# Performance work log

Hardware: AMD Instinct MI355X
Metric: run time of the kernel (lower is better)

The kernel has to match this reference:

```python
import jax, jax.numpy as jnp
import numpy as np

N = 8192        # nodes
D_IN = 256      # in_dims
D_OUT = 32      # out_dims (assignment clusters)


def setup_inputs() -> dict:
    key = jax.random.key(0)
    k1, k2, k3 = jax.random.split(key, 3)
    main_feat = jax.random.normal(k1, (N, D_IN), dtype=jnp.float32)
    main_adj = jax.random.uniform(k2, (N, N), dtype=jnp.float32)
    W = jax.random.normal(k3, (D_IN, D_OUT), dtype=jnp.float32) * (1.0 / np.sqrt(D_IN))
    b = jnp.zeros((D_OUT,), dtype=jnp.float32)
    return {"main_feat": main_feat, "main_adj": main_adj, "W": W, "b": b}


def reference(main_feat, main_adj, W, b):
    # GraphConvolution: support = X @ W ; out = A @ support + b   -> [N, D_OUT]
    support = main_feat @ W
    assign = main_adj @ support + b
    # softmax over the NODE axis (dim 0), matching F.softmax(main_assign, 0)
    assign = jax.nn.softmax(assign, axis=0)
    # pooling: raw_emb = assign^T @ X  -> [D_OUT, D_IN]
    raw_emb = assign.T @ main_feat
    return raw_emb
```

## Files before the change

### kernel.cpp

```cpp
#include <hip/hip_runtime.h>
#include <stdint.h>

#define NN   8192
#define DIN  256
#define DOUT 32

typedef short bf16x8 __attribute__((ext_vector_type(8)));
typedef float f32x16 __attribute__((ext_vector_type(16)));

union BF8 { uint32_t u[4]; bf16x8 v; };

__device__ __forceinline__ void split_pair(float a, float b, uint32_t& hp, uint32_t& lp) {
    uint32_t ua = __float_as_uint(a), ub = __float_as_uint(b);
    hp = (ua >> 16) | (ub & 0xffff0000u);
    float la = a - __uint_as_float(ua & 0xffff0000u);
    float lb = b - __uint_as_float(ub & 0xffff0000u);
    lp = (__float_as_uint(la) >> 16) | (__float_as_uint(lb) & 0xffff0000u);
}

__global__ __launch_bounds__(256) void k1_support(
    const float* __restrict__ X, const float* __restrict__ W,
    unsigned short* __restrict__ hi_frag, unsigned short* __restrict__ lo_frag)
{
    __shared__ float Xs[32 * 256];
    int t = threadIdx.x;
    int kbase = blockIdx.x * 32;

    const float4* Xg = (const float4*)(X + (size_t)kbase * DIN);
    float4* Xs4 = (float4*)Xs;
#pragma unroll
    for (int p = 0; p < 8; ++p) Xs4[p * 256 + t] = Xg[p * 256 + t];
    __syncthreads();

    int c = t & 31;
    int q = t >> 5;
    int kb2  = q >> 2;
    int half = (q >> 1) & 1;
    int j4   = q & 1;
    int krow0 = kb2 * 16 + half * 8 + j4 * 4;

    float acc[4] = {0.f, 0.f, 0.f, 0.f};
    for (int d = 0; d < 256; ++d) {
        float w = W[d * 32 + c];
#pragma unroll
        for (int jj = 0; jj < 4; ++jj)
            acc[jj] += Xs[(krow0 + jj) * 256 + d] * w;
    }

    uint32_t h01, l01, h23, l23;
    split_pair(acc[0], acc[1], h01, l01);
    split_pair(acc[2], acc[3], h23, l23);

    int ks = (kbase >> 4) + kb2;
    size_t elembase = (size_t)ks * 512 + (size_t)(half * 32 + c) * 8 + j4 * 4;
    *(uint2*)(hi_frag + elembase) = make_uint2(h01, h23);
    *(uint2*)(lo_frag + elembase) = make_uint2(l01, l23);
}

__global__ __launch_bounds__(256) void k2_logits(
    const float* __restrict__ adj,
    const unsigned short* __restrict__ hi_frag,
    const unsigned short* __restrict__ lo_frag,
    float* __restrict__ part)
{
    int t = threadIdx.x;
    int lane = t & 63, wv = t >> 6;
    int row_tile = blockIdx.x * 128 + wv * 32;
    int r  = lane & 31;
    int hs = lane >> 5;

    const float* arow = adj + (size_t)(row_tile + r) * NN + blockIdx.y * 512 + hs * 8;
    const unsigned short* hp = hi_frag + (size_t)blockIdx.y * 32 * 512 + lane * 8;
    const unsigned short* lp = lo_frag + (size_t)blockIdx.y * 32 * 512 + lane * 8;

    f32x16 acc;
#pragma unroll
    for (int i = 0; i < 16; ++i) acc[i] = 0.f;

#pragma unroll 4
    for (int s = 0; s < 32; ++s) {
        float4 a0 = *(const float4*)arow;
        float4 a1 = *(const float4*)(arow + 4);
        BF8 bh, bl, ah, al;
        bh.v = *(const bf16x8*)hp;
        bl.v = *(const bf16x8*)lp;
        split_pair(a0.x, a0.y, ah.u[0], al.u[0]);
        split_pair(a0.z, a0.w, ah.u[1], al.u[1]);
        split_pair(a1.x, a1.y, ah.u[2], al.u[2]);
        split_pair(a1.z, a1.w, ah.u[3], al.u[3]);
        acc = __builtin_amdgcn_mfma_f32_32x32x16_bf16(ah.v, bh.v, acc, 0, 0, 0);
        acc = __builtin_amdgcn_mfma_f32_32x32x16_bf16(ah.v, bl.v, acc, 0, 0, 0);
        acc = __builtin_amdgcn_mfma_f32_32x32x16_bf16(al.v, bh.v, acc, 0, 0, 0);
        arow += 16; hp += 512; lp += 512;
    }

    float* pdst = part + (size_t)blockIdx.y * (NN * DOUT);
#pragma unroll
    for (int reg = 0; reg < 16; ++reg) {
        int rt = (reg & 3) + 8 * (reg >> 2) + 4 * hs;
        pdst[(size_t)(row_tile + rt) * 32 + r] = acc[reg];
    }
}

__global__ __launch_bounds__(256) void k3a_sum_max(
    const float* __restrict__ part, float* __restrict__ logits_sum,
    float* __restrict__ Mpart)
{
    __shared__ float red[256 * 4];
    int t = threadIdx.x;
    size_t base4 = (size_t)blockIdx.x * 1024;

    float mx[4] = {-3.4e38f, -3.4e38f, -3.4e38f, -3.4e38f};
#pragma unroll
    for (int k = 0; k < 4; ++k) {
        size_t f = base4 + k * 256 + t;
        float4 v = ((const float4*)part)[f];
#pragma unroll
        for (int p = 1; p < 16; ++p) {
            float4 u = ((const float4*)(part + (size_t)p * NN * DOUT))[f];
            v.x += u.x; v.y += u.y; v.z += u.z; v.w += u.w;
        }
        ((float4*)logits_sum)[f] = v;
        mx[0] = fmaxf(mx[0], v.x); mx[1] = fmaxf(mx[1], v.y);
        mx[2] = fmaxf(mx[2], v.z); mx[3] = fmaxf(mx[3], v.w);
    }
#pragma unroll
    for (int j = 0; j < 4; ++j) red[t * 4 + j] = mx[j];
    __syncthreads();
    for (int s = 128; s >= 8; s >>= 1) {
        if (t < s)
#pragma unroll
            for (int j = 0; j < 4; ++j)
                red[t * 4 + j] = fmaxf(red[t * 4 + j], red[(t + s) * 4 + j]);
        __syncthreads();
    }
    if (t < 8)
#pragma unroll
        for (int j = 0; j < 4; ++j)
            Mpart[blockIdx.x * 32 + t * 4 + j] = red[t * 4 + j];
}

__global__ __launch_bounds__(256) void k3b_exp_sum(
    const float* __restrict__ logits_sum, const float* __restrict__ Mpart,
    float* __restrict__ e_buf, float* __restrict__ Spart)
{
    __shared__ float Ms[32];
    __shared__ float red[256 * 4];
    int t = threadIdx.x;

    if (t < 32) {
        float m = -3.4e38f;
        for (int g = 0; g < 64; ++g) m = fmaxf(m, Mpart[g * 32 + t]);
        Ms[t] = m;
    }
    __syncthreads();

    int g = t & 7;
    float m0 = Ms[4 * g], m1 = Ms[4 * g + 1], m2 = Ms[4 * g + 2], m3 = Ms[4 * g + 3];
    size_t base4 = (size_t)blockIdx.x * 1024;
    float sm[4] = {0.f, 0.f, 0.f, 0.f};
#pragma unroll
    for (int k = 0; k < 4; ++k) {
        size_t f = base4 + k * 256 + t;
        float4 v = ((const float4*)logits_sum)[f];
        v.x = __expf(v.x - m0); v.y = __expf(v.y - m1);
        v.z = __expf(v.z - m2); v.w = __expf(v.w - m3);
        ((float4*)e_buf)[f] = v;
        sm[0] += v.x; sm[1] += v.y; sm[2] += v.z; sm[3] += v.w;
    }
#pragma unroll
    for (int j = 0; j < 4; ++j) red[t * 4 + j] = sm[j];
    __syncthreads();
    for (int s = 128; s >= 8; s >>= 1) {
        if (t < s)
#pragma unroll
            for (int j = 0; j < 4; ++j)
                red[t * 4 + j] += red[(t + s) * 4 + j];
        __syncthreads();
    }
    if (t < 8)
#pragma unroll
        for (int j = 0; j < 4; ++j)
            Spart[blockIdx.x * 32 + t * 4 + j] = red[t * 4 + j];
}

__global__ __launch_bounds__(256) void k4_pool(
    const float* __restrict__ X, const float* __restrict__ e_buf,
    const float* __restrict__ Spart, float* __restrict__ p4)
{
    __shared__ float Xs[8 * 256];
    __shared__ float As[8 * 32];
    __shared__ float invS[32];
    int t = threadIdx.x;
    int c = t & 31, dg = t >> 5;
    int ibase = blockIdx.x * 64;

    if (t < 32) {
        float s = 0.f;
        for (int g = 0; g < 64; ++g) s += Spart[g * 32 + t];
        invS[t] = 1.0f / s;
    }

    float acc[32];
#pragma unroll
    for (int i = 0; i < 32; ++i) acc[i] = 0.f;

    for (int rnd = 0; rnd < 8; ++rnd) {
        __syncthreads();
        const float4* Xg = (const float4*)(X + (size_t)(ibase + rnd * 8) * DIN);
        float4* Xs4 = (float4*)Xs;
        Xs4[t]       = Xg[t];
        Xs4[256 + t] = Xg[256 + t];
        As[t] = e_buf[(size_t)(ibase + rnd * 8 + (t >> 5)) * 32 + (t & 31)] * invS[t & 31];
        __syncthreads();
#pragma unroll
        for (int i2 = 0; i2 < 8; ++i2) {
            float a = As[i2 * 32 + c];
#pragma unroll
            for (int dd = 0; dd < 32; ++dd)
                acc[dd] += a * Xs[i2 * 256 + dg * 32 + dd];
        }
    }
    float* dst = p4 + (size_t)blockIdx.x * (DOUT * DIN) + (size_t)c * 256 + dg * 32;
#pragma unroll
    for (int v = 0; v < 8; ++v)
        ((float4*)dst)[v] = make_float4(acc[v * 4], acc[v * 4 + 1], acc[v * 4 + 2], acc[v * 4 + 3]);
}

__global__ __launch_bounds__(256) void k5_reduce(
    const float* __restrict__ p4, float* __restrict__ out)
{
    int j = blockIdx.x * 256 + threadIdx.x;
    float a = 0.f;
    for (int g = 0; g < 128; ++g) a += p4[(size_t)g * (DOUT * DIN) + j];
    out[j] = a;
}

extern "C" void kernel_launch(void* const* d_in, const int* in_sizes, int n_in,
                              void* d_out, int out_size, void* d_ws, size_t ws_size,
                              hipStream_t stream) {
    const float* X   = (const float*)d_in[0];
    const float* adj = (const float*)d_in[1];
    const float* W   = (const float*)d_in[2];
    float* out = (float*)d_out;

    char* w = (char*)d_ws;
    unsigned short* hi_frag = (unsigned short*)w;
    unsigned short* lo_frag = (unsigned short*)(w + 512 * 1024);
    float* part       = (float*)(w + 1 * 1024 * 1024);
    float* logits_sum = (float*)(w + 17 * 1024 * 1024);
    float* e_buf      = (float*)(w + 18 * 1024 * 1024);
    float* Mpart      = (float*)(w + 19 * 1024 * 1024);
    float* Spart      = (float*)(w + 19 * 1024 * 1024 + 8192);
    float* p4         = (float*)(w + 19 * 1024 * 1024 + 16384);

    k1_support<<<NN / 32, 256, 0, stream>>>(X, W, hi_frag, lo_frag);
    k2_logits<<<dim3(NN / 128, 16), 256, 0, stream>>>(adj, hi_frag, lo_frag, part);
    k3a_sum_max<<<64, 256, 0, stream>>>(part, logits_sum, Mpart);
    k3b_exp_sum<<<64, 256, 0, stream>>>(logits_sum, Mpart, e_buf, Spart);
    k4_pool<<<128, 256, 0, stream>>>(X, e_buf, Spart, p4);
    k5_reduce<<<DOUT * DIN / 256, 256, 0, stream>>>(p4, out);
}
```

Baseline: 441.1 us.

## Restructure adjacency GEMM with LDS-staged coalesced tiles and rebalance reduction kernels

k2 now stages 32-row adjacency tiles through shared memory with register prefetch, so each wave reads contiguous rows with coalesced float4 loads. It uses 512-thread blocks that split the K range across 8 waves and reduce their accumulators in LDS, and it cuts the number of K-split partials from 16 to 4. The downstream softmax and pooling kernels get more blocks, padded partial strides to avoid channel or bank conflicts, and rotated read orders. The softmax normalization moves from k4 into the final reduce. In exchange there is extra LDS traffic, more barriers, and a larger cross-wave reduction in k2.

```diff
diff --git a/kernel.cpp b/kernel.cpp
--- a/kernel.cpp
+++ b/kernel.cpp
@@ -4,6 +4,9 @@
 #define NN   8192
 #define DIN  256
 #define DOUT 32
+
+#define PPART (NN * DOUT + 320)
+#define PP4   (DOUT * DIN + 320)
 
 typedef short bf16x8 __attribute__((ext_vector_type(8)));
 typedef float f32x16 __attribute__((ext_vector_type(16)));
@@ -57,48 +60,88 @@
     *(uint2*)(lo_frag + elembase) = make_uint2(l01, l23);
 }
 
-__global__ __launch_bounds__(256) void k2_logits(
+__global__ __launch_bounds__(512) void k2_logits(
     const float* __restrict__ adj,
     const unsigned short* __restrict__ hi_frag,
     const unsigned short* __restrict__ lo_frag,
     float* __restrict__ part)
 {
+    __shared__ __align__(16) float tile[32 * 260];
     int t = threadIdx.x;
     int lane = t & 63, wv = t >> 6;
-    int row_tile = blockIdx.x * 128 + wv * 32;
+    int row0 = blockIdx.x * 32;
+    size_t col0 = (size_t)blockIdx.y * 2048;
+
+    f32x16 acc;
+#pragma unroll
+    for (int i = 0; i < 16; ++i) acc[i] = 0.f;
+
     int r  = lane & 31;
     int hs = lane >> 5;
-
-    const float* arow = adj + (size_t)(row_tile + r) * NN + blockIdx.y * 512 + hs * 8;
-    const unsigned short* hp = hi_frag + (size_t)blockIdx.y * 32 * 512 + lane * 8;
-    const unsigned short* lp = lo_frag + (size_t)blockIdx.y * 32 * 512 + lane * 8;
-
-    f32x16 acc;
-#pragma unroll
-    for (int i = 0; i < 16; ++i) acc[i] = 0.f;
-
-#pragma unroll 4
-    for (int s = 0; s < 32; ++s) {
-        float4 a0 = *(const float4*)arow;
-        float4 a1 = *(const float4*)(arow + 4);
-        BF8 bh, bl, ah, al;
-        bh.v = *(const bf16x8*)hp;
-        bl.v = *(const bf16x8*)lp;
-        split_pair(a0.x, a0.y, ah.u[0], al.u[0]);
-        split_pair(a0.z, a0.w, ah.u[1], al.u[1]);
-        split_pair(a1.x, a1.y, ah.u[2], al.u[2]);
-        split_pair(a1.z, a1.w, ah.u[3], al.u[3]);
-        acc = __builtin_amdgcn_mfma_f32_32x32x16_bf16(ah.v, bh.v, acc, 0, 0, 0);
-        acc = __builtin_amdgcn_mfma_f32_32x32x16_bf16(ah.v, bl.v, acc, 0, 0, 0);
-        acc = __builtin_amdgcn_mfma_f32_32x32x16_bf16(al.v, bh.v, acc, 0, 0, 0);
-        arow += 16; hp += 512; lp += 512;
-    }
-
-    float* pdst = part + (size_t)blockIdx.y * (NN * DOUT);
-#pragma unroll
-    for (int reg = 0; reg < 16; ++reg) {
-        int rt = (reg & 3) + 8 * (reg >> 2) + 4 * hs;
-        pdst[(size_t)(row_tile + rt) * 32 + r] = acc[reg];
+    int tl0 = blockIdx.x & 7;
+
+    const float* asrc = adj + (size_t)(row0 + wv) * NN + col0 + lane * 4;
+
+    float4 pref[4];
+    {
+#pragma unroll
+        for (int p = 0; p < 4; ++p)
+            pref[p] = *(const float4*)(asrc + (size_t)(8 * p) * NN + tl0 * 256);
+#pragma unroll
+        for (int p = 0; p < 4; ++p)
+            *(float4*)((char*)tile + (wv + 8 * p) * 1040 + lane * 16) = pref[p];
+    }
+
+    for (int tt = 0; tt < 8; ++tt) {
+        int tl  = (tt + tl0) & 7;
+        int tln = (tt + 1 + tl0) & 7;
+        if (tt < 7) {
+#pragma unroll
+            for (int p = 0; p < 4; ++p)
+                pref[p] = *(const float4*)(asrc + (size_t)(8 * p) * NN + tln * 256);
+        }
+        __syncthreads();
+#pragma unroll
+        for (int ss = 0; ss < 2; ++ss) {
+            int s = 2 * wv + ss;
+            const float4* ap = (const float4*)((const char*)tile + r * 1040 + s * 64 + hs * 32);
+            float4 a0 = ap[0];
+            float4 a1 = ap[1];
+            int ks = (int)blockIdx.y * 128 + tl * 16 + s;
+            BF8 bh, bl, ah, al;
+            bh.v = *(const bf16x8*)(hi_frag + (size_t)ks * 512 + lane * 8);
+            bl.v = *(const bf16x8*)(lo_frag + (size_t)ks * 512 + lane * 8);
+            split_pair(a0.x, a0.y, ah.u[0], al.u[0]);
+            split_pair(a0.z, a0.w, ah.u[1], al.u[1]);
+            split_pair(a1.x, a1.y, ah.u[2], al.u[2]);
+            split_pair(a1.z, a1.w, ah.u[3], al.u[3]);
+            acc = __builtin_amdgcn_mfma_f32_32x32x16_bf16(ah.v, bh.v, acc, 0, 0, 0);
+            acc = __builtin_amdgcn_mfma_f32_32x32x16_bf16(ah.v, bl.v, acc, 0, 0, 0);
+            acc = __builtin_amdgcn_mfma_f32_32x32x16_bf16(al.v, bh.v, acc, 0, 0, 0);
+        }
+        if (tt < 7) {
+            __syncthreads();
+#pragma unroll
+            for (int p = 0; p < 4; ++p)
+                *(float4*)((char*)tile + (wv + 8 * p) * 1040 + lane * 16) = pref[p];
+        }
+    }
+
+    __syncthreads();
+    float* red = tile;
+#pragma unroll
+    for (int g = 0; g < 16; ++g) red[wv * 1024 + lane * 16 + g] = acc[g];
+    __syncthreads();
+
+    float* pdst = part + (size_t)blockIdx.y * PPART + (size_t)row0 * 32;
+    for (int a = t; a < 1024; a += 512) {
+        int row = a >> 5, colc = a & 31;
+        int l = colc + 32 * ((row >> 2) & 1);
+        int g = (row & 3) | ((row >> 3) << 2);
+        float ssum = 0.f;
+#pragma unroll
+        for (int w8 = 0; w8 < 8; ++w8) ssum += red[w8 * 1024 + l * 16 + g];
+        pdst[a] = ssum;
     }
 }
 
@@ -108,24 +151,19 @@
 {
     __shared__ float red[256 * 4];
     int t = threadIdx.x;
-    size_t base4 = (size_t)blockIdx.x * 1024;
-
-    float mx[4] = {-3.4e38f, -3.4e38f, -3.4e38f, -3.4e38f};
-#pragma unroll
-    for (int k = 0; k < 4; ++k) {
-        size_t f = base4 + k * 256 + t;
-        float4 v = ((const float4*)part)[f];
-#pragma unroll
-        for (int p = 1; p < 16; ++p) {
-            float4 u = ((const float4*)(part + (size_t)p * NN * DOUT))[f];
-            v.x += u.x; v.y += u.y; v.z += u.z; v.w += u.w;
-        }
-        ((float4*)logits_sum)[f] = v;
-        mx[0] = fmaxf(mx[0], v.x); mx[1] = fmaxf(mx[1], v.y);
-        mx[2] = fmaxf(mx[2], v.z); mx[3] = fmaxf(mx[3], v.w);
-    }
-#pragma unroll
-    for (int j = 0; j < 4; ++j) red[t * 4 + j] = mx[j];
+    size_t f = (size_t)blockIdx.x * 256 + t;
+
+    float4 v = make_float4(0.f, 0.f, 0.f, 0.f);
+#pragma unroll
+    for (int pp = 0; pp < 4; ++pp) {
+        int p = (pp + blockIdx.x) & 3;
+        float4 u = ((const float4*)(part + (size_t)p * PPART))[f];
+        v.x += u.x; v.y += u.y; v.z += u.z; v.w += u.w;
+    }
+    ((float4*)logits_sum)[f] = v;
+
+    red[t * 4 + 0] = v.x; red[t * 4 + 1] = v.y;
+    red[t * 4 + 2] = v.z; red[t * 4 + 3] = v.w;
     __syncthreads();
     for (int s = 128; s >= 8; s >>= 1) {
         if (t < s)
@@ -144,32 +182,32 @@
     const float* __restrict__ logits_sum, const float* __restrict__ Mpart,
     float* __restrict__ e_buf, float* __restrict__ Spart)
 {
-    __shared__ float Ms[32];
     __shared__ float red[256 * 4];
     int t = threadIdx.x;
-
-    if (t < 32) {
-        float m = -3.4e38f;
-        for (int g = 0; g < 64; ++g) m = fmaxf(m, Mpart[g * 32 + t]);
-        Ms[t] = m;
-    }
-    __syncthreads();
-
-    int g = t & 7;
-    float m0 = Ms[4 * g], m1 = Ms[4 * g + 1], m2 = Ms[4 * g + 2], m3 = Ms[4 * g + 3];
-    size_t base4 = (size_t)blockIdx.x * 1024;
-    float sm[4] = {0.f, 0.f, 0.f, 0.f};
-#pragma unroll
-    for (int k = 0; k < 4; ++k) {
-        size_t f = base4 + k * 256 + t;
-        float4 v = ((const float4*)logits_sum)[f];
-        v.x = __expf(v.x - m0); v.y = __expf(v.y - m1);
-        v.z = __expf(v.z - m2); v.w = __expf(v.w - m3);
-        ((float4*)e_buf)[f] = v;
-        sm[0] += v.x; sm[1] += v.y; sm[2] += v.z; sm[3] += v.w;
-    }
-#pragma unroll
-    for (int j = 0; j < 4; ++j) red[t * 4 + j] = sm[j];
+    int c = t & 31, g0 = t >> 5;
+
+    float m = -3.4e38f;
+#pragma unroll
+    for (int gg = 0; gg < 32; ++gg)
+        m = fmaxf(m, Mpart[(g0 * 32 + gg) * 32 + c]);
+    red[t] = m;
+    __syncthreads();
+    for (int s = 128; s >= 32; s >>= 1) {
+        if (t < s) red[t] = fmaxf(red[t], red[t + s]);
+        __syncthreads();
+    }
+    float m0 = red[(4 * t + 0) & 31], m1 = red[(4 * t + 1) & 31];
+    float m2 = red[(4 * t + 2) & 31], m3 = red[(4 * t + 3) & 31];
+    __syncthreads();
+
+    size_t f = (size_t)blockIdx.x * 256 + t;
+    float4 v = ((const float4*)logits_sum)[f];
+    v.x = __expf(v.x - m0); v.y = __expf(v.y - m1);
+    v.z = __expf(v.z - m2); v.w = __expf(v.w - m3);
+    ((float4*)e_buf)[f] = v;
+
+    red[t * 4 + 0] = v.x; red[t * 4 + 1] = v.y;
+    red[t * 4 + 2] = v.z; red[t * 4 + 3] = v.w;
     __syncthreads();
     for (int s = 128; s >= 8; s >>= 1) {
         if (t < s)
@@ -186,32 +224,25 @@
 
 __global__ __launch_bounds__(256) void k4_pool(
     const float* __restrict__ X, const float* __restrict__ e_buf,
-    const float* __restrict__ Spart, float* __restrict__ p4)
+    float* __restrict__ p4)
 {
     __shared__ float Xs[8 * 256];
     __shared__ float As[8 * 32];
-    __shared__ float invS[32];
     int t = threadIdx.x;
     int c = t & 31, dg = t >> 5;
-    int ibase = blockIdx.x * 64;
-
-    if (t < 32) {
-        float s = 0.f;
-        for (int g = 0; g < 64; ++g) s += Spart[g * 32 + t];
-        invS[t] = 1.0f / s;
-    }
+    int ibase = blockIdx.x * 32;
 
     float acc[32];
 #pragma unroll
     for (int i = 0; i < 32; ++i) acc[i] = 0.f;
 
-    for (int rnd = 0; rnd < 8; ++rnd) {
+    for (int rnd = 0; rnd < 4; ++rnd) {
         __syncthreads();
         const float4* Xg = (const float4*)(X + (size_t)(ibase + rnd * 8) * DIN);
         float4* Xs4 = (float4*)Xs;
         Xs4[t]       = Xg[t];
         Xs4[256 + t] = Xg[256 + t];
-        As[t] = e_buf[(size_t)(ibase + rnd * 8 + (t >> 5)) * 32 + (t & 31)] * invS[t & 31];
+        As[t] = e_buf[(size_t)(ibase + rnd * 8 + (t >> 5)) * 32 + (t & 31)];
         __syncthreads();
 #pragma unroll
         for (int i2 = 0; i2 < 8; ++i2) {
@@ -221,19 +252,43 @@
                 acc[dd] += a * Xs[i2 * 256 + dg * 32 + dd];
         }
     }
-    float* dst = p4 + (size_t)blockIdx.x * (DOUT * DIN) + (size_t)c * 256 + dg * 32;
+    float* dst = p4 + (size_t)blockIdx.x * PP4 + (size_t)c * 256 + dg * 32;
 #pragma unroll
     for (int v = 0; v < 8; ++v)
         ((float4*)dst)[v] = make_float4(acc[v * 4], acc[v * 4 + 1], acc[v * 4 + 2], acc[v * 4 + 3]);
 }
 
 __global__ __launch_bounds__(256) void k5_reduce(
-    const float* __restrict__ p4, float* __restrict__ out)
-{
-    int j = blockIdx.x * 256 + threadIdx.x;
+    const float* __restrict__ p4, const float* __restrict__ Spart,
+    float* __restrict__ out)
+{
+    __shared__ float red[256];
+    __shared__ float sred[256];
+    int t = threadIdx.x;
+    int c_out = blockIdx.x >> 3;
+
+    sred[t] = Spart[t * 32 + c_out];
+
+    int j = blockIdx.x * 32 + (t & 31);
+    int g0 = t >> 5;
     float a = 0.f;
-    for (int g = 0; g < 128; ++g) a += p4[(size_t)g * (DOUT * DIN) + j];
-    out[j] = a;
+#pragma unroll
+    for (int gg = 0; gg < 32; ++gg) {
+        int g = (g0 * 32 + gg + blockIdx.x) & 255;
+        a += p4[(size_t)g * PP4 + j];
+    }
+    red[t] = a;
+    __syncthreads();
+    for (int s = 128; s >= 32; s >>= 1) {
+        if (t < s) { red[t] += red[t + s]; sred[t] += sred[t + s]; }
+        __syncthreads();
+    }
+    if (t < 32) {
+        float sv = sred[t];
+#pragma unroll
+        for (int off = 16; off >= 1; off >>= 1) sv += __shfl_xor(sv, off);
+        out[blockIdx.x * 32 + t] = red[t] / sv;
+    }
 }
 
 extern "C" void kernel_launch(void* const* d_in, const int* in_sizes, int n_in,
@@ -247,17 +302,18 @@
     char* w = (char*)d_ws;
     unsigned short* hi_frag = (unsigned short*)w;
     unsigned short* lo_frag = (unsigned short*)(w + 512 * 1024);
-    float* part       = (float*)(w + 1 * 1024 * 1024);
-    float* logits_sum = (float*)(w + 17 * 1024 * 1024);
-    float* e_buf      = (float*)(w + 18 * 1024 * 1024);
-    float* Mpart      = (float*)(w + 19 * 1024 * 1024);
-    float* Spart      = (float*)(w + 19 * 1024 * 1024 + 8192);
-    float* p4         = (float*)(w + 19 * 1024 * 1024 + 16384);
+    size_t off = 1024 * 1024;
+    float* part = (float*)(w + off);            off += (size_t)4 * PPART * sizeof(float);
+    float* logits_sum = (float*)(w + off);      off += (size_t)NN * DOUT * sizeof(float);
+    float* e_buf = (float*)(w + off);           off += (size_t)NN * DOUT * sizeof(float);
+    float* Mpart = (float*)(w + off);           off += 256 * 32 * sizeof(float);
+    float* Spart = (float*)(w + off);           off += 256 * 32 * sizeof(float);
+    float* p4 = (float*)(w + off);              off += (size_t)256 * PP4 * sizeof(float);
 
     k1_support<<<NN / 32, 256, 0, stream>>>(X, W, hi_frag, lo_frag);
-    k2_logits<<<dim3(NN / 128, 16), 256, 0, stream>>>(adj, hi_frag, lo_frag, part);
-    k3a_sum_max<<<64, 256, 0, stream>>>(part, logits_sum, Mpart);
-    k3b_exp_sum<<<64, 256, 0, stream>>>(logits_sum, Mpart, e_buf, Spart);
-    k4_pool<<<128, 256, 0, stream>>>(X, e_buf, Spart, p4);
-    k5_reduce<<<DOUT * DIN / 256, 256, 0, stream>>>(p4, out);
-}
+    k2_logits<<<dim3(NN / 32, 4), 512, 0, stream>>>(adj, hi_frag, lo_frag, part);
+    k3a_sum_max<<<256, 256, 0, stream>>>(part, logits_sum, Mpart);
+    k3b_exp_sum<<<256, 256, 0, stream>>>(logits_sum, Mpart, e_buf, Spart);
+    k4_pool<<<256, 256, 0, stream>>>(X, e_buf, p4);
+    k5_reduce<<<256, 256, 0, stream>>>(p4, Spart, out);
+}
```

Result: no change. 448.9 us (+1.8%).
